# Kernel optimization log

Measured on AMD Instinct MI355X. Metric: run time of the kernel, lower is better.

Reference implementation:

```python
import jax, jax.numpy as jnp
import numpy as np

N = 1_000_000   # total nodes
B = 1024        # number of graphs
H = 64          # node feature dim / LSTM hidden
STEPS = 5       # Set2Set processing steps
PROJ = 128      # projection_dim


def setup_inputs() -> dict:
    key = jax.random.key(0)
    ks = jax.random.split(key, 12)
    x = jax.random.normal(ks[0], (N, H), dtype=jnp.float32)
    batch = jnp.sort(jax.random.randint(ks[1], (N,), 0, B)).astype(jnp.int64)
    s = 1.0 / np.sqrt(H)
    # torch.nn.LSTM(input_size=2H, hidden_size=H), gate order i,f,g,o
    W_ih = jax.random.uniform(ks[2], (4 * H, 2 * H), minval=-s, maxval=s, dtype=jnp.float32)
    W_hh = jax.random.uniform(ks[3], (4 * H, H), minval=-s, maxval=s, dtype=jnp.float32)
    b_ih = jax.random.uniform(ks[4], (4 * H,), minval=-s, maxval=s, dtype=jnp.float32)
    b_hh = jax.random.uniform(ks[5], (4 * H,), minval=-s, maxval=s, dtype=jnp.float32)
    s1 = 1.0 / np.sqrt(2 * H)
    W1 = jax.random.uniform(ks[6], (256, 2 * H), minval=-s1, maxval=s1, dtype=jnp.float32)
    b1 = jax.random.uniform(ks[7], (256,), minval=-s1, maxval=s1, dtype=jnp.float32)
    s2 = 1.0 / np.sqrt(256)
    W2 = jax.random.uniform(ks[8], (PROJ, 256), minval=-s2, maxval=s2, dtype=jnp.float32)
    b2 = jax.random.uniform(ks[9], (PROJ,), minval=-s2, maxval=s2, dtype=jnp.float32)
    return {"x": x, "batch": batch, "W_ih": W_ih, "W_hh": W_hh, "b_ih": b_ih,
            "b_hh": b_hh, "W1": W1, "b1": b1, "W2": W2, "b2": b2}


def _set2set(x, batch, W_ih, W_hh, b_ih, b_hh):
    q_star = jnp.zeros((B, 2 * H), x.dtype)
    h = jnp.zeros((B, H), x.dtype)
    c = jnp.zeros((B, H), x.dtype)
    for _ in range(STEPS):
        gates = q_star @ W_ih.T + b_ih + h @ W_hh.T + b_hh
        i, f, g, o = jnp.split(gates, 4, axis=-1)
        i = jax.nn.sigmoid(i); f = jax.nn.sigmoid(f)
        g = jnp.tanh(g); o = jax.nn.sigmoid(o)
        c = f * c + i * g
        h = o * jnp.tanh(c)
        q = h  # [B, H]
        # segment-wise attention over ragged node sets
        e = jnp.sum(x * q[batch], axis=-1)                         # [N]
        emax = jax.ops.segment_max(e, batch, num_segments=B)       # [B]
        a = jnp.exp(e - emax[batch])
        denom = jax.ops.segment_sum(a, batch, num_segments=B)
        a = a / jnp.maximum(denom, 1e-16)[batch]
        r = jax.ops.segment_sum(a[:, None] * x, batch, num_segments=B)  # [B, H]
        q_star = jnp.concatenate([q, r], axis=-1)
    return q_star


def reference(x, batch, W_ih, W_hh, b_ih, b_hh, W1, b1, W2, b2):
    out = _set2set(x, batch, W_ih, W_hh, b_ih, b_hh)   # [B, 2H]
    out = out @ W1.T + b1                               # [B, 256]
    out = jax.nn.relu(out) @ W2.T + b2                  # [B, PROJ]
    return out
```

## Files before the change

### kernel.cpp

```cpp
#include <hip/hip_runtime.h>
#include <float.h>
#include <math.h>

#define NB 1024
#define HD 64
#define NSTEPS 5
#define SPLIT 4

__device__ __forceinline__ float sigmoidf_(float x) {
    return 1.0f / (1.0f + __expf(-x));
}

__global__ void seg_bounds_kernel(const int* __restrict__ batch,
                                  int* __restrict__ seg_start, int n) {
    int i = blockIdx.x * blockDim.x + threadIdx.x;
    if (i >= n) return;
    int b = batch[i];
    if (i == 0) {
        for (int j = 0; j <= b; ++j) seg_start[j] = 0;
    } else {
        int pb = batch[i - 1];
        for (int j = pb + 1; j <= b; ++j) seg_start[j] = i;
    }
    if (i == n - 1) {
        for (int j = b + 1; j <= NB; ++j) seg_start[j] = n;
    }
}

__global__ void lstm_kernel(const float* __restrict__ W_ih,
                            const float* __restrict__ W_hh,
                            const float* __restrict__ b_ih,
                            const float* __restrict__ b_hh,
                            const float* __restrict__ pm,
                            const float* __restrict__ ps,
                            const float* __restrict__ pr,
                            float* __restrict__ h,
                            float* __restrict__ c,
                            int first) {
    const int G = 8;
    int g0 = blockIdx.x * G;
    __shared__ float s_qs[G][128];
    __shared__ float s_gates[G][256];
    int tid = threadIdx.x;

    if (!first) {
        for (int idx = tid; idx < G * 64; idx += 256) {
            int g = idx >> 6, k = idx & 63;
            s_qs[g][k] = h[(g0 + g) * 64 + k];
        }
        for (int idx = tid; idx < G * 64; idx += 256) {
            int g = idx >> 6, k = idx & 63;
            int b = g0 + g;
            float m0 = pm[b * SPLIT + 0], m1 = pm[b * SPLIT + 1];
            float m2 = pm[b * SPLIT + 2], m3 = pm[b * SPLIT + 3];
            float M = fmaxf(fmaxf(m0, m1), fmaxf(m2, m3));
            float w0 = __expf(m0 - M), w1 = __expf(m1 - M);
            float w2 = __expf(m2 - M), w3 = __expf(m3 - M);
            float S = ps[b * SPLIT + 0] * w0 + ps[b * SPLIT + 1] * w1
                    + ps[b * SPLIT + 2] * w2 + ps[b * SPLIT + 3] * w3;
            float rf = pr[(b * SPLIT + 0) * 64 + k] * w0
                     + pr[(b * SPLIT + 1) * 64 + k] * w1
                     + pr[(b * SPLIT + 2) * 64 + k] * w2
                     + pr[(b * SPLIT + 3) * 64 + k] * w3;
            s_qs[g][64 + k] = rf / fmaxf(S, 1e-16f);
        }
        __syncthreads();
    }

    int j = tid;
    float acc[G];
    float bias = b_ih[j] + b_hh[j];
#pragma unroll
    for (int g = 0; g < G; ++g) acc[g] = bias;

    if (!first) {
        const float4* wih = (const float4*)(W_ih + j * 128);
#pragma unroll 4
        for (int k4 = 0; k4 < 32; ++k4) {
            float4 w = wih[k4];
#pragma unroll
            for (int g = 0; g < G; ++g) {
                acc[g] = fmaf(w.x, s_qs[g][k4 * 4 + 0], acc[g]);
                acc[g] = fmaf(w.y, s_qs[g][k4 * 4 + 1], acc[g]);
                acc[g] = fmaf(w.z, s_qs[g][k4 * 4 + 2], acc[g]);
                acc[g] = fmaf(w.w, s_qs[g][k4 * 4 + 3], acc[g]);
            }
        }
        const float4* whh = (const float4*)(W_hh + j * 64);
#pragma unroll 4
        for (int k4 = 0; k4 < 16; ++k4) {
            float4 w = whh[k4];
#pragma unroll
            for (int g = 0; g < G; ++g) {
                acc[g] = fmaf(w.x, s_qs[g][k4 * 4 + 0], acc[g]);
                acc[g] = fmaf(w.y, s_qs[g][k4 * 4 + 1], acc[g]);
                acc[g] = fmaf(w.z, s_qs[g][k4 * 4 + 2], acc[g]);
                acc[g] = fmaf(w.w, s_qs[g][k4 * 4 + 3], acc[g]);
            }
        }
    }
#pragma unroll
    for (int g = 0; g < G; ++g) s_gates[g][j] = acc[g];
    __syncthreads();

    for (int idx = tid; idx < G * 64; idx += 256) {
        int g = idx >> 6, jj = idx & 63;
        int gb = g0 + g;
        float ig = sigmoidf_(s_gates[g][jj]);
        float fg = sigmoidf_(s_gates[g][jj + 64]);
        float gg = tanhf(s_gates[g][jj + 128]);
        float og = sigmoidf_(s_gates[g][jj + 192]);
        float cprev = first ? 0.0f : c[gb * 64 + jj];
        float cn = fmaf(fg, cprev, ig * gg);
        float hn = og * tanhf(cn);
        c[gb * 64 + jj] = cn;
        h[gb * 64 + jj] = hn;
    }
}

__global__ __launch_bounds__(256) void attn_kernel(const float* __restrict__ x,
                                                   const int* __restrict__ seg_start,
                                                   const float* __restrict__ h,
                                                   float* __restrict__ pm,
                                                   float* __restrict__ ps,
                                                   float* __restrict__ pr) {
    int bs = blockIdx.x;
    int b = bs >> 2;
    int slice = bs & (SPLIT - 1);
    int s0 = seg_start[b], e0 = seg_start[b + 1];
    int len = e0 - s0;
    int s = s0 + (int)(((long long)len * slice) >> 2);
    int e = s0 + (int)(((long long)len * (slice + 1)) >> 2);

    int tid = threadIdx.x;
    int lane = tid & 63;
    int wave = tid >> 6;
    int fc = lane & 15;
    int grp = lane >> 4;

    float4 q4 = *(const float4*)(h + b * 64 + fc * 4);

    float m = -FLT_MAX, sum = 0.0f;
    float4 r4 = make_float4(0.0f, 0.0f, 0.0f, 0.0f);

    const int maxidx4 = e * 16 - 1;
    for (int base = s + wave * 16; base < e; base += 64) {
#pragma unroll
        for (int t = 0; t < 4; ++t) {
            int node = base + t * 4 + grp;
            int idx4 = base * 16 + t * 64 + lane;
            idx4 = min(idx4, maxidx4);
            float4 xv = *(const float4*)(x + (size_t)idx4 * 4);

            float d = xv.x * q4.x;
            d = fmaf(xv.y, q4.y, d);
            d = fmaf(xv.z, q4.z, d);
            d = fmaf(xv.w, q4.w, d);
            d += __shfl_xor(d, 1);
            d += __shfl_xor(d, 2);
            d += __shfl_xor(d, 4);
            d += __shfl_xor(d, 8);

            bool valid = node < e;
            float eeff = valid ? d : -FLT_MAX;
            float nm = fmaxf(m, eeff);
            float sc = __expf(m - nm);
            float w = valid ? __expf(eeff - nm) : 0.0f;
            sum = fmaf(sum, sc, w);
            r4.x = fmaf(r4.x, sc, w * xv.x);
            r4.y = fmaf(r4.y, sc, w * xv.y);
            r4.z = fmaf(r4.z, sc, w * xv.z);
            r4.w = fmaf(r4.w, sc, w * xv.w);
            m = nm;
        }
    }

#pragma unroll
    for (int off = 16; off < 64; off <<= 1) {
        float om = __shfl_xor(m, off);
        float os = __shfl_xor(sum, off);
        float ox = __shfl_xor(r4.x, off);
        float oy = __shfl_xor(r4.y, off);
        float oz = __shfl_xor(r4.z, off);
        float ow = __shfl_xor(r4.w, off);
        float nm = fmaxf(m, om);
        float s1 = __expf(m - nm);
        float s2 = __expf(om - nm);
        sum = sum * s1 + os * s2;
        r4.x = r4.x * s1 + ox * s2;
        r4.y = r4.y * s1 + oy * s2;
        r4.z = r4.z * s1 + oz * s2;
        r4.w = r4.w * s1 + ow * s2;
        m = nm;
    }

    __shared__ float lm[4], ls[4], lr[4][64];
    if (lane < 16) {
        if (lane == 0) { lm[wave] = m; ls[wave] = sum; }
        *(float4*)&lr[wave][lane * 4] = r4;
    }
    __syncthreads();
    if (tid < 64) {
        float M = fmaxf(fmaxf(lm[0], lm[1]), fmaxf(lm[2], lm[3]));
        float w0 = __expf(lm[0] - M), w1 = __expf(lm[1] - M);
        float w2 = __expf(lm[2] - M), w3 = __expf(lm[3] - M);
        float S = ls[0] * w0 + ls[1] * w1 + ls[2] * w2 + ls[3] * w3;
        float rf = lr[0][tid] * w0 + lr[1][tid] * w1 + lr[2][tid] * w2 + lr[3][tid] * w3;
        if (tid == 0) { pm[bs] = M; ps[bs] = S; }
        pr[bs * 64 + tid] = rf;
    }
}

__global__ void mlp_kernel(const float* __restrict__ h,
                           const float* __restrict__ pm,
                           const float* __restrict__ ps,
                           const float* __restrict__ pr,
                           const float* __restrict__ W1,
                           const float* __restrict__ b1,
                           const float* __restrict__ W2,
                           const float* __restrict__ b2,
                           float* __restrict__ out) {
    int b = blockIdx.x;
    __shared__ float qs[128];
    __shared__ float hid[256];
    int tid = threadIdx.x;
    if (tid < 64) {
        qs[tid] = h[b * 64 + tid];
    } else if (tid < 128) {
        int k = tid - 64;
        float m0 = pm[b * SPLIT + 0], m1 = pm[b * SPLIT + 1];
        float m2 = pm[b * SPLIT + 2], m3 = pm[b * SPLIT + 3];
        float M = fmaxf(fmaxf(m0, m1), fmaxf(m2, m3));
        float w0 = __expf(m0 - M), w1 = __expf(m1 - M);
        float w2 = __expf(m2 - M), w3 = __expf(m3 - M);
        float S = ps[b * SPLIT + 0] * w0 + ps[b * SPLIT + 1] * w1
                + ps[b * SPLIT + 2] * w2 + ps[b * SPLIT + 3] * w3;
        float rf = pr[(b * SPLIT + 0) * 64 + k] * w0
                 + pr[(b * SPLIT + 1) * 64 + k] * w1
                 + pr[(b * SPLIT + 2) * 64 + k] * w2
                 + pr[(b * SPLIT + 3) * 64 + k] * w3;
        qs[tid] = rf / fmaxf(S, 1e-16f);
    }
    __syncthreads();
    float acc = b1[tid];
    const float4* w = (const float4*)(W1 + tid * 128);
#pragma unroll 4
    for (int k4 = 0; k4 < 32; ++k4) {
        float4 ww = w[k4];
        acc = fmaf(ww.x, qs[k4 * 4 + 0], acc);
        acc = fmaf(ww.y, qs[k4 * 4 + 1], acc);
        acc = fmaf(ww.z, qs[k4 * 4 + 2], acc);
        acc = fmaf(ww.w, qs[k4 * 4 + 3], acc);
    }
    hid[tid] = fmaxf(acc, 0.0f);
    __syncthreads();
    if (tid < 128) {
        float acc2 = b2[tid];
        const float4* w2 = (const float4*)(W2 + tid * 256);
#pragma unroll 4
        for (int k4 = 0; k4 < 64; ++k4) {
            float4 ww = w2[k4];
            acc2 = fmaf(ww.x, hid[k4 * 4 + 0], acc2);
            acc2 = fmaf(ww.y, hid[k4 * 4 + 1], acc2);
            acc2 = fmaf(ww.z, hid[k4 * 4 + 2], acc2);
            acc2 = fmaf(ww.w, hid[k4 * 4 + 3], acc2);
        }
        out[b * 128 + tid] = acc2;
    }
}

extern "C" void kernel_launch(void* const* d_in, const int* in_sizes, int n_in,
                              void* d_out, int out_size, void* d_ws, size_t ws_size,
                              hipStream_t stream) {
    const float* x    = (const float*)d_in[0];
    const int*   batch= (const int*)d_in[1];
    const float* W_ih = (const float*)d_in[2];
    const float* W_hh = (const float*)d_in[3];
    const float* b_ih = (const float*)d_in[4];
    const float* b_hh = (const float*)d_in[5];
    const float* W1   = (const float*)d_in[6];
    const float* b1   = (const float*)d_in[7];
    const float* W2   = (const float*)d_in[8];
    const float* b2   = (const float*)d_in[9];
    float* out = (float*)d_out;
    const int N = in_sizes[1];

    float* h   = (float*)d_ws;
    float* c   = h + NB * 64;
    int*   seg = (int*)(c + NB * 64);
    float* pm  = (float*)(seg + NB + 8);
    float* ps  = pm + NB * SPLIT;
    float* pr  = ps + NB * SPLIT;

    seg_bounds_kernel<<<(N + 255) / 256, 256, 0, stream>>>(batch, seg, N);

    for (int step = 0; step < NSTEPS; ++step) {
        lstm_kernel<<<NB / 8, 256, 0, stream>>>(W_ih, W_hh, b_ih, b_hh,
                                                pm, ps, pr, h, c, step == 0 ? 1 : 0);
        attn_kernel<<<NB * SPLIT, 256, 0, stream>>>(x, seg, h, pm, ps, pr);
    }
    mlp_kernel<<<NB, 256, 0, stream>>>(h, pm, ps, pr, W1, b1, W2, b2, out);
}
```

Baseline: 614.6 us.

## Fuse all stages into one cooperative persistent kernel with grid syncs

Replaces the sequence of separate seg-bounds, LSTM, attention and MLP launches with a single cooperative kernel of 1024 blocks. Stages are separated by grid.sync(), which removes per-launch overhead. The attention step drops the 4-way split per graph, so each graph is handled by one block and writes a normalized r directly, with no partial-merge pass. This leaves fewer blocks to stream x (1024 instead of 4096), and occupancy must allow all 1024 blocks to be co-resident, otherwise it falls back to the multi-kernel path.

```diff
diff --git a/kernel.cpp b/kernel.cpp
--- a/kernel.cpp
+++ b/kernel.cpp
@@ -1,14 +1,239 @@
 #include <hip/hip_runtime.h>
+#include <hip/hip_cooperative_groups.h>
 #include <float.h>
 #include <math.h>
 
+namespace cg = cooperative_groups;
+
 #define NB 1024
-#define HD 64
 #define NSTEPS 5
 #define SPLIT 4
 
 __device__ __forceinline__ float sigmoidf_(float x) {
     return 1.0f / (1.0f + __expf(-x));
+}
+
+union SharedU {
+    struct { float qs[8][128]; float gates[8][256]; } lstm;
+    struct { float lm[4]; float ls[4]; float lr[4][64]; } attn;
+    struct { float qs[128]; float hid[256]; } mlp;
+};
+
+__global__ __launch_bounds__(256, 4) void mega_kernel(
+    const float* __restrict__ x, const int* __restrict__ batch, int N,
+    const float* __restrict__ W_ih, const float* __restrict__ W_hh,
+    const float* __restrict__ b_ih, const float* __restrict__ b_hh,
+    const float* __restrict__ W1, const float* __restrict__ b1,
+    const float* __restrict__ W2, const float* __restrict__ b2,
+    float* __restrict__ h, float* __restrict__ c, float* __restrict__ rbuf,
+    int* __restrict__ seg, float* __restrict__ out)
+{
+    cg::grid_group grid = cg::this_grid();
+    __shared__ SharedU sh;
+    const int blk = blockIdx.x, tid = threadIdx.x;
+
+    if (blk >= 128) {
+        for (int i = (blk - 128) * 256 + tid; i < N; i += 896 * 256) {
+            int b = batch[i];
+            if (i == 0) { for (int j = 0; j <= b; ++j) seg[j] = 0; }
+            else { int pb = batch[i - 1]; for (int j = pb + 1; j <= b; ++j) seg[j] = i; }
+            if (i == N - 1) { for (int j = b + 1; j <= NB; ++j) seg[j] = N; }
+        }
+    } else {
+        int g0 = blk * 8;
+        sh.lstm.gates[0][tid] = b_ih[tid] + b_hh[tid];
+        __syncthreads();
+        for (int idx = tid; idx < 8 * 64; idx += 256) {
+            int g = idx >> 6, jj = idx & 63;
+            int gb = g0 + g;
+            float ig = sigmoidf_(sh.lstm.gates[0][jj]);
+            float fg = sigmoidf_(sh.lstm.gates[0][jj + 64]);
+            float gg = tanhf(sh.lstm.gates[0][jj + 128]);
+            float og = sigmoidf_(sh.lstm.gates[0][jj + 192]);
+            (void)fg;
+            float cn = ig * gg;
+            float hn = og * tanhf(cn);
+            c[gb * 64 + jj] = cn;
+            h[gb * 64 + jj] = hn;
+        }
+    }
+    grid.sync();
+
+    for (int step = 0; ; ++step) {
+        {
+            const int b = blk;
+            const int s = seg[b], e = seg[b + 1];
+            const int lane = tid & 63;
+            const int wave = tid >> 6;
+            const int fc = lane & 15;
+            const int grp = lane >> 4;
+
+            float4 q4 = *(const float4*)(h + b * 64 + fc * 4);
+
+            float m = -FLT_MAX, sum = 0.0f;
+            float4 r4 = make_float4(0.0f, 0.0f, 0.0f, 0.0f);
+
+            const int maxidx4 = e * 16 - 1;
+            for (int base = s + wave * 16; base < e; base += 64) {
+#pragma unroll
+                for (int t = 0; t < 4; ++t) {
+                    int node = base + t * 4 + grp;
+                    int idx4 = base * 16 + t * 64 + lane;
+                    idx4 = min(idx4, maxidx4);
+                    float4 xv = *(const float4*)(x + (size_t)idx4 * 4);
+
+                    float d = xv.x * q4.x;
+                    d = fmaf(xv.y, q4.y, d);
+                    d = fmaf(xv.z, q4.z, d);
+                    d = fmaf(xv.w, q4.w, d);
+                    d += __shfl_xor(d, 1);
+                    d += __shfl_xor(d, 2);
+                    d += __shfl_xor(d, 4);
+                    d += __shfl_xor(d, 8);
+
+                    bool valid = node < e;
+                    float eeff = valid ? d : -FLT_MAX;
+                    float nm = fmaxf(m, eeff);
+                    float sc = __expf(m - nm);
+                    float w = valid ? __expf(eeff - nm) : 0.0f;
+                    sum = fmaf(sum, sc, w);
+                    r4.x = fmaf(r4.x, sc, w * xv.x);
+                    r4.y = fmaf(r4.y, sc, w * xv.y);
+                    r4.z = fmaf(r4.z, sc, w * xv.z);
+                    r4.w = fmaf(r4.w, sc, w * xv.w);
+                    m = nm;
+                }
+            }
+
+#pragma unroll
+            for (int off = 16; off < 64; off <<= 1) {
+                float om = __shfl_xor(m, off);
+                float os = __shfl_xor(sum, off);
+                float ox = __shfl_xor(r4.x, off);
+                float oy = __shfl_xor(r4.y, off);
+                float oz = __shfl_xor(r4.z, off);
+                float ow = __shfl_xor(r4.w, off);
+                float nm = fmaxf(m, om);
+                float s1 = __expf(m - nm);
+                float s2 = __expf(om - nm);
+                sum = sum * s1 + os * s2;
+                r4.x = r4.x * s1 + ox * s2;
+                r4.y = r4.y * s1 + oy * s2;
+                r4.z = r4.z * s1 + oz * s2;
+                r4.w = r4.w * s1 + ow * s2;
+                m = nm;
+            }
+
+            __syncthreads();
+            if (lane < 16) {
+                if (lane == 0) { sh.attn.lm[wave] = m; sh.attn.ls[wave] = sum; }
+                *(float4*)&sh.attn.lr[wave][lane * 4] = r4;
+            }
+            __syncthreads();
+            if (tid < 64) {
+                float M = fmaxf(fmaxf(sh.attn.lm[0], sh.attn.lm[1]),
+                                fmaxf(sh.attn.lm[2], sh.attn.lm[3]));
+                float w0 = __expf(sh.attn.lm[0] - M), w1 = __expf(sh.attn.lm[1] - M);
+                float w2 = __expf(sh.attn.lm[2] - M), w3 = __expf(sh.attn.lm[3] - M);
+                float S = sh.attn.ls[0] * w0 + sh.attn.ls[1] * w1
+                        + sh.attn.ls[2] * w2 + sh.attn.ls[3] * w3;
+                float rf = sh.attn.lr[0][tid] * w0 + sh.attn.lr[1][tid] * w1
+                         + sh.attn.lr[2][tid] * w2 + sh.attn.lr[3][tid] * w3;
+                rbuf[b * 64 + tid] = rf / fmaxf(S, 1e-16f);
+            }
+        }
+        if (step == NSTEPS - 1) break;
+        grid.sync();
+
+        if (blk < 128) {
+            int g0 = blk * 8;
+            for (int idx = tid; idx < 8 * 64; idx += 256) {
+                int g = idx >> 6, k = idx & 63;
+                sh.lstm.qs[g][k] = h[(g0 + g) * 64 + k];
+                sh.lstm.qs[g][64 + k] = rbuf[(g0 + g) * 64 + k];
+            }
+            __syncthreads();
+
+            float acc[8];
+            float bias = b_ih[tid] + b_hh[tid];
+#pragma unroll
+            for (int g = 0; g < 8; ++g) acc[g] = bias;
+            const float4* wih = (const float4*)(W_ih + tid * 128);
+#pragma unroll 4
+            for (int k4 = 0; k4 < 32; ++k4) {
+                float4 w = wih[k4];
+#pragma unroll
+                for (int g = 0; g < 8; ++g) {
+                    acc[g] = fmaf(w.x, sh.lstm.qs[g][k4 * 4 + 0], acc[g]);
+                    acc[g] = fmaf(w.y, sh.lstm.qs[g][k4 * 4 + 1], acc[g]);
+                    acc[g] = fmaf(w.z, sh.lstm.qs[g][k4 * 4 + 2], acc[g]);
+                    acc[g] = fmaf(w.w, sh.lstm.qs[g][k4 * 4 + 3], acc[g]);
+                }
+            }
+            const float4* whh = (const float4*)(W_hh + tid * 64);
+#pragma unroll 4
+            for (int k4 = 0; k4 < 16; ++k4) {
+                float4 w = whh[k4];
+#pragma unroll
+                for (int g = 0; g < 8; ++g) {
+                    acc[g] = fmaf(w.x, sh.lstm.qs[g][k4 * 4 + 0], acc[g]);
+                    acc[g] = fmaf(w.y, sh.lstm.qs[g][k4 * 4 + 1], acc[g]);
+                    acc[g] = fmaf(w.z, sh.lstm.qs[g][k4 * 4 + 2], acc[g]);
+                    acc[g] = fmaf(w.w, sh.lstm.qs[g][k4 * 4 + 3], acc[g]);
+                }
+            }
+#pragma unroll
+            for (int g = 0; g < 8; ++g) sh.lstm.gates[g][tid] = acc[g];
+            __syncthreads();
+
+            for (int idx = tid; idx < 8 * 64; idx += 256) {
+                int g = idx >> 6, jj = idx & 63;
+                int gb = g0 + g;
+                float ig = sigmoidf_(sh.lstm.gates[g][jj]);
+                float fg = sigmoidf_(sh.lstm.gates[g][jj + 64]);
+                float gg = tanhf(sh.lstm.gates[g][jj + 128]);
+                float og = sigmoidf_(sh.lstm.gates[g][jj + 192]);
+                float cn = fmaf(fg, c[gb * 64 + jj], ig * gg);
+                float hn = og * tanhf(cn);
+                c[gb * 64 + jj] = cn;
+                h[gb * 64 + jj] = hn;
+            }
+        }
+        grid.sync();
+    }
+
+    __syncthreads();
+    {
+        const int b = blk;
+        if (tid < 64) sh.mlp.qs[tid] = h[b * 64 + tid];
+        else if (tid < 128) sh.mlp.qs[tid] = rbuf[b * 64 + (tid - 64)];
+        __syncthreads();
+        float acc = b1[tid];
+        const float4* w = (const float4*)(W1 + tid * 128);
+#pragma unroll 4
+        for (int k4 = 0; k4 < 32; ++k4) {
+            float4 ww = w[k4];
+            acc = fmaf(ww.x, sh.mlp.qs[k4 * 4 + 0], acc);
+            acc = fmaf(ww.y, sh.mlp.qs[k4 * 4 + 1], acc);
+            acc = fmaf(ww.z, sh.mlp.qs[k4 * 4 + 2], acc);
+            acc = fmaf(ww.w, sh.mlp.qs[k4 * 4 + 3], acc);
+        }
+        sh.mlp.hid[tid] = fmaxf(acc, 0.0f);
+        __syncthreads();
+        if (tid < 128) {
+            float acc2 = b2[tid];
+            const float4* w2 = (const float4*)(W2 + tid * 256);
+#pragma unroll 4
+            for (int k4 = 0; k4 < 64; ++k4) {
+                float4 ww = w2[k4];
+                acc2 = fmaf(ww.x, sh.mlp.hid[k4 * 4 + 0], acc2);
+                acc2 = fmaf(ww.y, sh.mlp.hid[k4 * 4 + 1], acc2);
+                acc2 = fmaf(ww.z, sh.mlp.hid[k4 * 4 + 2], acc2);
+                acc2 = fmaf(ww.w, sh.mlp.hid[k4 * 4 + 3], acc2);
+            }
+            out[b * 128 + tid] = acc2;
+        }
+    }
 }
 
 __global__ void seg_bounds_kernel(const int* __restrict__ batch,
@@ -16,63 +241,33 @@
     int i = blockIdx.x * blockDim.x + threadIdx.x;
     if (i >= n) return;
     int b = batch[i];
-    if (i == 0) {
-        for (int j = 0; j <= b; ++j) seg_start[j] = 0;
-    } else {
-        int pb = batch[i - 1];
-        for (int j = pb + 1; j <= b; ++j) seg_start[j] = i;
-    }
-    if (i == n - 1) {
-        for (int j = b + 1; j <= NB; ++j) seg_start[j] = n;
-    }
-}
-
-__global__ void lstm_kernel(const float* __restrict__ W_ih,
-                            const float* __restrict__ W_hh,
-                            const float* __restrict__ b_ih,
-                            const float* __restrict__ b_hh,
-                            const float* __restrict__ pm,
-                            const float* __restrict__ ps,
-                            const float* __restrict__ pr,
-                            float* __restrict__ h,
-                            float* __restrict__ c,
-                            int first) {
+    if (i == 0) { for (int j = 0; j <= b; ++j) seg_start[j] = 0; }
+    else { int pb = batch[i - 1]; for (int j = pb + 1; j <= b; ++j) seg_start[j] = i; }
+    if (i == n - 1) { for (int j = b + 1; j <= NB; ++j) seg_start[j] = n; }
+}
+
+__global__ void lstm_kernel_fb(const float* __restrict__ W_ih, const float* __restrict__ W_hh,
+                               const float* __restrict__ b_ih, const float* __restrict__ b_hh,
+                               const float* __restrict__ rbuf,
+                               float* __restrict__ h, float* __restrict__ c, int first) {
     const int G = 8;
     int g0 = blockIdx.x * G;
     __shared__ float s_qs[G][128];
     __shared__ float s_gates[G][256];
     int tid = threadIdx.x;
-
     if (!first) {
         for (int idx = tid; idx < G * 64; idx += 256) {
             int g = idx >> 6, k = idx & 63;
             s_qs[g][k] = h[(g0 + g) * 64 + k];
-        }
-        for (int idx = tid; idx < G * 64; idx += 256) {
-            int g = idx >> 6, k = idx & 63;
-            int b = g0 + g;
-            float m0 = pm[b * SPLIT + 0], m1 = pm[b * SPLIT + 1];
-            float m2 = pm[b * SPLIT + 2], m3 = pm[b * SPLIT + 3];
-            float M = fmaxf(fmaxf(m0, m1), fmaxf(m2, m3));
-            float w0 = __expf(m0 - M), w1 = __expf(m1 - M);
-            float w2 = __expf(m2 - M), w3 = __expf(m3 - M);
-            float S = ps[b * SPLIT + 0] * w0 + ps[b * SPLIT + 1] * w1
-                    + ps[b * SPLIT + 2] * w2 + ps[b * SPLIT + 3] * w3;
-            float rf = pr[(b * SPLIT + 0) * 64 + k] * w0
-                     + pr[(b * SPLIT + 1) * 64 + k] * w1
-                     + pr[(b * SPLIT + 2) * 64 + k] * w2
-                     + pr[(b * SPLIT + 3) * 64 + k] * w3;
-            s_qs[g][64 + k] = rf / fmaxf(S, 1e-16f);
+            s_qs[g][64 + k] = rbuf[(g0 + g) * 64 + k];
         }
         __syncthreads();
     }
-
     int j = tid;
     float acc[G];
     float bias = b_ih[j] + b_hh[j];
 #pragma unroll
     for (int g = 0; g < G; ++g) acc[g] = bias;
-
     if (!first) {
         const float4* wih = (const float4*)(W_ih + j * 128);
 #pragma unroll 4
@@ -102,7 +297,6 @@
 #pragma unroll
     for (int g = 0; g < G; ++g) s_gates[g][j] = acc[g];
     __syncthreads();
-
     for (int idx = tid; idx < G * 64; idx += 256) {
         int g = idx >> 6, jj = idx & 63;
         int gb = g0 + g;
@@ -118,31 +312,20 @@
     }
 }
 
-__global__ __launch_bounds__(256) void attn_kernel(const float* __restrict__ x,
-                                                   const int* __restrict__ seg_start,
-                                                   const float* __restrict__ h,
-                                                   float* __restrict__ pm,
-                                                   float* __restrict__ ps,
-                                                   float* __restrict__ pr) {
-    int bs = blockIdx.x;
-    int b = bs >> 2;
-    int slice = bs & (SPLIT - 1);
-    int s0 = seg_start[b], e0 = seg_start[b + 1];
-    int len = e0 - s0;
-    int s = s0 + (int)(((long long)len * slice) >> 2);
-    int e = s0 + (int)(((long long)len * (slice + 1)) >> 2);
-
+__global__ __launch_bounds__(256) void attn_kernel_fb(const float* __restrict__ x,
+                                                      const int* __restrict__ seg_start,
+                                                      const float* __restrict__ h,
+                                                      float* __restrict__ rbuf) {
+    int b = blockIdx.x;
+    int s = seg_start[b], e = seg_start[b + 1];
     int tid = threadIdx.x;
     int lane = tid & 63;
     int wave = tid >> 6;
     int fc = lane & 15;
     int grp = lane >> 4;
-
     float4 q4 = *(const float4*)(h + b * 64 + fc * 4);
-
     float m = -FLT_MAX, sum = 0.0f;
     float4 r4 = make_float4(0.0f, 0.0f, 0.0f, 0.0f);
-
     const int maxidx4 = e * 16 - 1;
     for (int base = s + wave * 16; base < e; base += 64) {
 #pragma unroll
@@ -151,7 +334,6 @@
             int idx4 = base * 16 + t * 64 + lane;
             idx4 = min(idx4, maxidx4);
             float4 xv = *(const float4*)(x + (size_t)idx4 * 4);
-
             float d = xv.x * q4.x;
             d = fmaf(xv.y, q4.y, d);
             d = fmaf(xv.z, q4.z, d);
@@ -160,7 +342,6 @@
             d += __shfl_xor(d, 2);
             d += __shfl_xor(d, 4);
             d += __shfl_xor(d, 8);
-
             bool valid = node < e;
             float eeff = valid ? d : -FLT_MAX;
             float nm = fmaxf(m, eeff);
@@ -174,7 +355,6 @@
             m = nm;
         }
     }
-
 #pragma unroll
     for (int off = 16; off < 64; off <<= 1) {
         float om = __shfl_xor(m, off);
@@ -193,7 +373,6 @@
         r4.w = r4.w * s1 + ow * s2;
         m = nm;
     }
-
     __shared__ float lm[4], ls[4], lr[4][64];
     if (lane < 16) {
         if (lane == 0) { lm[wave] = m; ls[wave] = sum; }
@@ -206,41 +385,20 @@
         float w2 = __expf(lm[2] - M), w3 = __expf(lm[3] - M);
         float S = ls[0] * w0 + ls[1] * w1 + ls[2] * w2 + ls[3] * w3;
         float rf = lr[0][tid] * w0 + lr[1][tid] * w1 + lr[2][tid] * w2 + lr[3][tid] * w3;
-        if (tid == 0) { pm[bs] = M; ps[bs] = S; }
-        pr[bs * 64 + tid] = rf;
-    }
-}
-
-__global__ void mlp_kernel(const float* __restrict__ h,
-                           const float* __restrict__ pm,
-                           const float* __restrict__ ps,
-                           const float* __restrict__ pr,
-                           const float* __restrict__ W1,
-                           const float* __restrict__ b1,
-                           const float* __restrict__ W2,
-                           const float* __restrict__ b2,
-                           float* __restrict__ out) {
+        rbuf[b * 64 + tid] = rf / fmaxf(S, 1e-16f);
+    }
+}
+
+__global__ void mlp_kernel_fb(const float* __restrict__ h, const float* __restrict__ rbuf,
+                              const float* __restrict__ W1, const float* __restrict__ b1,
+                              const float* __restrict__ W2, const float* __restrict__ b2,
+                              float* __restrict__ out) {
     int b = blockIdx.x;
     __shared__ float qs[128];
     __shared__ float hid[256];
     int tid = threadIdx.x;
-    if (tid < 64) {
-        qs[tid] = h[b * 64 + tid];
-    } else if (tid < 128) {
-        int k = tid - 64;
-        float m0 = pm[b * SPLIT + 0], m1 = pm[b * SPLIT + 1];
-        float m2 = pm[b * SPLIT + 2], m3 = pm[b * SPLIT + 3];
-        float M = fmaxf(fmaxf(m0, m1), fmaxf(m2, m3));
-        float w0 = __expf(m0 - M), w1 = __expf(m1 - M);
-        float w2 = __expf(m2 - M), w3 = __expf(m3 - M);
-        float S = ps[b * SPLIT + 0] * w0 + ps[b * SPLIT + 1] * w1
-                + ps[b * SPLIT + 2] * w2 + ps[b * SPLIT + 3] * w3;
-        float rf = pr[(b * SPLIT + 0) * 64 + k] * w0
-                 + pr[(b * SPLIT + 1) * 64 + k] * w1
-                 + pr[(b * SPLIT + 2) * 64 + k] * w2
-                 + pr[(b * SPLIT + 3) * 64 + k] * w3;
-        qs[tid] = rf / fmaxf(S, 1e-16f);
-    }
+    if (tid < 64) qs[tid] = h[b * 64 + tid];
+    else if (tid < 128) qs[tid] = rbuf[b * 64 + (tid - 64)];
     __syncthreads();
     float acc = b1[tid];
     const float4* w = (const float4*)(W1 + tid * 128);
@@ -283,21 +441,28 @@
     const float* W2   = (const float*)d_in[8];
     const float* b2   = (const float*)d_in[9];
     float* out = (float*)d_out;
-    const int N = in_sizes[1];
-
-    float* h   = (float*)d_ws;
-    float* c   = h + NB * 64;
-    int*   seg = (int*)(c + NB * 64);
-    float* pm  = (float*)(seg + NB + 8);
-    float* ps  = pm + NB * SPLIT;
-    float* pr  = ps + NB * SPLIT;
-
-    seg_bounds_kernel<<<(N + 255) / 256, 256, 0, stream>>>(batch, seg, N);
-
-    for (int step = 0; step < NSTEPS; ++step) {
-        lstm_kernel<<<NB / 8, 256, 0, stream>>>(W_ih, W_hh, b_ih, b_hh,
-                                                pm, ps, pr, h, c, step == 0 ? 1 : 0);
-        attn_kernel<<<NB * SPLIT, 256, 0, stream>>>(x, seg, h, pm, ps, pr);
-    }
-    mlp_kernel<<<NB, 256, 0, stream>>>(h, pm, ps, pr, W1, b1, W2, b2, out);
-}
+    int N = in_sizes[1];
+
+    float* h    = (float*)d_ws;
+    float* c    = h + NB * 64;
+    float* rbuf = c + NB * 64;
+    int*   seg  = (int*)(rbuf + NB * 64);
+
+    void* args[] = {
+        (void*)&x, (void*)&batch, (void*)&N,
+        (void*)&W_ih, (void*)&W_hh, (void*)&b_ih, (void*)&b_hh,
+        (void*)&W1, (void*)&b1, (void*)&W2, (void*)&b2,
+        (void*)&h, (void*)&c, (void*)&rbuf, (void*)&seg, (void*)&out
+    };
+    hipError_t err = hipLaunchCooperativeKernel((void*)mega_kernel, dim3(NB), dim3(256),
+                                                args, 0, stream);
+    if (err != hipSuccess) {
+        seg_bounds_kernel<<<(N + 255) / 256, 256, 0, stream>>>(batch, seg, N);
+        for (int step = 0; step < NSTEPS; ++step) {
+            lstm_kernel_fb<<<NB / 8, 256, 0, stream>>>(W_ih, W_hh, b_ih, b_hh,
+                                                       rbuf, h, c, step == 0 ? 1 : 0);
+            attn_kernel_fb<<<NB, 256, 0, stream>>>(x, seg, h, rbuf);
+        }
+        mlp_kernel_fb<<<NB, 256, 0, stream>>>(h, rbuf, W1, b1, W2, b2, out);
+    }
+}
```

Result: slower. 1.622 ms (+163.9%).

## Use one block per graph with register double-buffered x prefetch in attention

Applied to the files above, without the earlier changes.

Drops the 4-way split of each graph across blocks, so the attention kernel handles a whole segment per block and writes the normalized readout directly. This removes the partial max/sum/readout buffers and the merge logic in the LSTM and MLP kernels. The node loop now loads 32 nodes per wave and prefetches the next chunk into registers while computing the current one, to raise memory-level parallelism. The grid becomes four times smaller and each wave uses more registers, which risks lower occupancy and load imbalance.

```diff
diff --git a/kernel.cpp b/kernel.cpp
--- a/kernel.cpp
+++ b/kernel.cpp
@@ -3,9 +3,7 @@
 #include <math.h>
 
 #define NB 1024
-#define HD 64
 #define NSTEPS 5
-#define SPLIT 4
 
 __device__ __forceinline__ float sigmoidf_(float x) {
     return 1.0f / (1.0f + __expf(-x));
@@ -16,63 +14,33 @@
     int i = blockIdx.x * blockDim.x + threadIdx.x;
     if (i >= n) return;
     int b = batch[i];
-    if (i == 0) {
-        for (int j = 0; j <= b; ++j) seg_start[j] = 0;
-    } else {
-        int pb = batch[i - 1];
-        for (int j = pb + 1; j <= b; ++j) seg_start[j] = i;
-    }
-    if (i == n - 1) {
-        for (int j = b + 1; j <= NB; ++j) seg_start[j] = n;
-    }
-}
-
-__global__ void lstm_kernel(const float* __restrict__ W_ih,
-                            const float* __restrict__ W_hh,
-                            const float* __restrict__ b_ih,
-                            const float* __restrict__ b_hh,
-                            const float* __restrict__ pm,
-                            const float* __restrict__ ps,
-                            const float* __restrict__ pr,
-                            float* __restrict__ h,
-                            float* __restrict__ c,
-                            int first) {
+    if (i == 0) { for (int j = 0; j <= b; ++j) seg_start[j] = 0; }
+    else { int pb = batch[i - 1]; for (int j = pb + 1; j <= b; ++j) seg_start[j] = i; }
+    if (i == n - 1) { for (int j = b + 1; j <= NB; ++j) seg_start[j] = n; }
+}
+
+__global__ void lstm_kernel(const float* __restrict__ W_ih, const float* __restrict__ W_hh,
+                            const float* __restrict__ b_ih, const float* __restrict__ b_hh,
+                            const float* __restrict__ rbuf,
+                            float* __restrict__ h, float* __restrict__ c, int first) {
     const int G = 8;
     int g0 = blockIdx.x * G;
     __shared__ float s_qs[G][128];
     __shared__ float s_gates[G][256];
     int tid = threadIdx.x;
-
     if (!first) {
         for (int idx = tid; idx < G * 64; idx += 256) {
             int g = idx >> 6, k = idx & 63;
             s_qs[g][k] = h[(g0 + g) * 64 + k];
-        }
-        for (int idx = tid; idx < G * 64; idx += 256) {
-            int g = idx >> 6, k = idx & 63;
-            int b = g0 + g;
-            float m0 = pm[b * SPLIT + 0], m1 = pm[b * SPLIT + 1];
-            float m2 = pm[b * SPLIT + 2], m3 = pm[b * SPLIT + 3];
-            float M = fmaxf(fmaxf(m0, m1), fmaxf(m2, m3));
-            float w0 = __expf(m0 - M), w1 = __expf(m1 - M);
-            float w2 = __expf(m2 - M), w3 = __expf(m3 - M);
-            float S = ps[b * SPLIT + 0] * w0 + ps[b * SPLIT + 1] * w1
-                    + ps[b * SPLIT + 2] * w2 + ps[b * SPLIT + 3] * w3;
-            float rf = pr[(b * SPLIT + 0) * 64 + k] * w0
-                     + pr[(b * SPLIT + 1) * 64 + k] * w1
-                     + pr[(b * SPLIT + 2) * 64 + k] * w2
-                     + pr[(b * SPLIT + 3) * 64 + k] * w3;
-            s_qs[g][64 + k] = rf / fmaxf(S, 1e-16f);
+            s_qs[g][64 + k] = rbuf[(g0 + g) * 64 + k];
         }
         __syncthreads();
     }
-
     int j = tid;
     float acc[G];
     float bias = b_ih[j] + b_hh[j];
 #pragma unroll
     for (int g = 0; g < G; ++g) acc[g] = bias;
-
     if (!first) {
         const float4* wih = (const float4*)(W_ih + j * 128);
 #pragma unroll 4
@@ -102,7 +70,6 @@
 #pragma unroll
     for (int g = 0; g < G; ++g) s_gates[g][j] = acc[g];
     __syncthreads();
-
     for (int idx = tid; idx < G * 64; idx += 256) {
         int g = idx >> 6, jj = idx & 63;
         int gb = g0 + g;
@@ -121,17 +88,9 @@
 __global__ __launch_bounds__(256) void attn_kernel(const float* __restrict__ x,
                                                    const int* __restrict__ seg_start,
                                                    const float* __restrict__ h,
-                                                   float* __restrict__ pm,
-                                                   float* __restrict__ ps,
-                                                   float* __restrict__ pr) {
-    int bs = blockIdx.x;
-    int b = bs >> 2;
-    int slice = bs & (SPLIT - 1);
-    int s0 = seg_start[b], e0 = seg_start[b + 1];
-    int len = e0 - s0;
-    int s = s0 + (int)(((long long)len * slice) >> 2);
-    int e = s0 + (int)(((long long)len * (slice + 1)) >> 2);
-
+                                                   float* __restrict__ rbuf) {
+    int b = blockIdx.x;
+    int s = seg_start[b], e = seg_start[b + 1];
     int tid = threadIdx.x;
     int lane = tid & 63;
     int wave = tid >> 6;
@@ -144,34 +103,55 @@
     float4 r4 = make_float4(0.0f, 0.0f, 0.0f, 0.0f);
 
     const int maxidx4 = e * 16 - 1;
-    for (int base = s + wave * 16; base < e; base += 64) {
-#pragma unroll
-        for (int t = 0; t < 4; ++t) {
-            int node = base + t * 4 + grp;
-            int idx4 = base * 16 + t * 64 + lane;
-            idx4 = min(idx4, maxidx4);
-            float4 xv = *(const float4*)(x + (size_t)idx4 * 4);
-
-            float d = xv.x * q4.x;
-            d = fmaf(xv.y, q4.y, d);
-            d = fmaf(xv.z, q4.z, d);
-            d = fmaf(xv.w, q4.w, d);
-            d += __shfl_xor(d, 1);
-            d += __shfl_xor(d, 2);
-            d += __shfl_xor(d, 4);
-            d += __shfl_xor(d, 8);
-
-            bool valid = node < e;
-            float eeff = valid ? d : -FLT_MAX;
-            float nm = fmaxf(m, eeff);
-            float sc = __expf(m - nm);
-            float w = valid ? __expf(eeff - nm) : 0.0f;
-            sum = fmaf(sum, sc, w);
-            r4.x = fmaf(r4.x, sc, w * xv.x);
-            r4.y = fmaf(r4.y, sc, w * xv.y);
-            r4.z = fmaf(r4.z, sc, w * xv.z);
-            r4.w = fmaf(r4.w, sc, w * xv.w);
-            m = nm;
+    int pos = s + wave * 32;
+
+    if (pos < e) {
+        float4 cur[8];
+#pragma unroll
+        for (int t = 0; t < 8; ++t) {
+            int idx4 = min(pos * 16 + t * 64 + lane, maxidx4);
+            cur[t] = *(const float4*)(x + (size_t)idx4 * 4);
+        }
+        while (true) {
+            int pos2 = pos + 128;
+            bool more = (pos2 < e);
+            float4 nxt[8];
+            if (more) {
+#pragma unroll
+                for (int t = 0; t < 8; ++t) {
+                    int idx4 = min(pos2 * 16 + t * 64 + lane, maxidx4);
+                    nxt[t] = *(const float4*)(x + (size_t)idx4 * 4);
+                }
+            }
+#pragma unroll
+            for (int t = 0; t < 8; ++t) {
+                int node = pos + t * 4 + grp;
+                float4 xv = cur[t];
+                float d = xv.x * q4.x;
+                d = fmaf(xv.y, q4.y, d);
+                d = fmaf(xv.z, q4.z, d);
+                d = fmaf(xv.w, q4.w, d);
+                d += __shfl_xor(d, 1);
+                d += __shfl_xor(d, 2);
+                d += __shfl_xor(d, 4);
+                d += __shfl_xor(d, 8);
+
+                bool valid = node < e;
+                float eeff = valid ? d : -FLT_MAX;
+                float nm = fmaxf(m, eeff);
+                float sc = __expf(m - nm);
+                float w = valid ? __expf(eeff - nm) : 0.0f;
+                sum = fmaf(sum, sc, w);
+                r4.x = fmaf(r4.x, sc, w * xv.x);
+                r4.y = fmaf(r4.y, sc, w * xv.y);
+                r4.z = fmaf(r4.z, sc, w * xv.z);
+                r4.w = fmaf(r4.w, sc, w * xv.w);
+                m = nm;
+            }
+            if (!more) break;
+            pos = pos2;
+#pragma unroll
+            for (int t = 0; t < 8; ++t) cur[t] = nxt[t];
         }
     }
 
@@ -206,41 +186,20 @@
         float w2 = __expf(lm[2] - M), w3 = __expf(lm[3] - M);
         float S = ls[0] * w0 + ls[1] * w1 + ls[2] * w2 + ls[3] * w3;
         float rf = lr[0][tid] * w0 + lr[1][tid] * w1 + lr[2][tid] * w2 + lr[3][tid] * w3;
-        if (tid == 0) { pm[bs] = M; ps[bs] = S; }
-        pr[bs * 64 + tid] = rf;
-    }
-}
-
-__global__ void mlp_kernel(const float* __restrict__ h,
-                           const float* __restrict__ pm,
-                           const float* __restrict__ ps,
-                           const float* __restrict__ pr,
-                           const float* __restrict__ W1,
-                           const float* __restrict__ b1,
-                           const float* __restrict__ W2,
-                           const float* __restrict__ b2,
+        rbuf[b * 64 + tid] = rf / fmaxf(S, 1e-16f);
+    }
+}
+
+__global__ void mlp_kernel(const float* __restrict__ h, const float* __restrict__ rbuf,
+                           const float* __restrict__ W1, const float* __restrict__ b1,
+                           const float* __restrict__ W2, const float* __restrict__ b2,
                            float* __restrict__ out) {
     int b = blockIdx.x;
     __shared__ float qs[128];
     __shared__ float hid[256];
     int tid = threadIdx.x;
-    if (tid < 64) {
-        qs[tid] = h[b * 64 + tid];
-    } else if (tid < 128) {
-        int k = tid - 64;
-        float m0 = pm[b * SPLIT + 0], m1 = pm[b * SPLIT + 1];
-        float m2 = pm[b * SPLIT + 2], m3 = pm[b * SPLIT + 3];
-        float M = fmaxf(fmaxf(m0, m1), fmaxf(m2, m3));
-        float w0 = __expf(m0 - M), w1 = __expf(m1 - M);
-        float w2 = __expf(m2 - M), w3 = __expf(m3 - M);
-        float S = ps[b * SPLIT + 0] * w0 + ps[b * SPLIT + 1] * w1
-                + ps[b * SPLIT + 2] * w2 + ps[b * SPLIT + 3] * w3;
-        float rf = pr[(b * SPLIT + 0) * 64 + k] * w0
-                 + pr[(b * SPLIT + 1) * 64 + k] * w1
-                 + pr[(b * SPLIT + 2) * 64 + k] * w2
-                 + pr[(b * SPLIT + 3) * 64 + k] * w3;
-        qs[tid] = rf / fmaxf(S, 1e-16f);
-    }
+    if (tid < 64) qs[tid] = h[b * 64 + tid];
+    else if (tid < 128) qs[tid] = rbuf[b * 64 + (tid - 64)];
     __syncthreads();
     float acc = b1[tid];
     const float4* w = (const float4*)(W1 + tid * 128);
@@ -283,21 +242,18 @@
     const float* W2   = (const float*)d_in[8];
     const float* b2   = (const float*)d_in[9];
     float* out = (float*)d_out;
-    const int N = in_sizes[1];
-
-    float* h   = (float*)d_ws;
-    float* c   = h + NB * 64;
-    int*   seg = (int*)(c + NB * 64);
-    float* pm  = (float*)(seg + NB + 8);
-    float* ps  = pm + NB * SPLIT;
-    float* pr  = ps + NB * SPLIT;
+    int N = in_sizes[1];
+
+    float* h    = (float*)d_ws;
+    float* c    = h + NB * 64;
+    float* rbuf = c + NB * 64;
+    int*   seg  = (int*)(rbuf + NB * 64);
 
     seg_bounds_kernel<<<(N + 255) / 256, 256, 0, stream>>>(batch, seg, N);
-
     for (int step = 0; step < NSTEPS; ++step) {
         lstm_kernel<<<NB / 8, 256, 0, stream>>>(W_ih, W_hh, b_ih, b_hh,
-                                                pm, ps, pr, h, c, step == 0 ? 1 : 0);
-        attn_kernel<<<NB * SPLIT, 256, 0, stream>>>(x, seg, h, pm, ps, pr);
-    }
-    mlp_kernel<<<NB, 256, 0, stream>>>(h, pm, ps, pr, W1, b1, W2, b2, out);
-}
+                                                rbuf, h, c, step == 0 ? 1 : 0);
+        attn_kernel<<<NB, 256, 0, stream>>>(x, seg, h, rbuf);
+    }
+    mlp_kernel<<<NB, 256, 0, stream>>>(h, rbuf, W1, b1, W2, b2, out);
+}
```

After: 626.9 us. 2.0% more time.
